# Performance work log

Hardware: AMD Instinct MI355X
Metric: run time of the kernel (lower is better)

The kernel has to match this reference:

```python
import jax, jax.numpy as jnp
import numpy as np

T, B, N, F = 128, 8, 32, 128
H = 256  # hidden channels
DEG = 8


def setup_inputs() -> dict:
    key = jax.random.key(0)
    ks = jax.random.split(key, 8)
    data = jax.random.normal(ks[0], (T, B, N, F), jnp.float32)
    all_ohs = jax.random.normal(ks[1], (T, B, N, 8), jnp.float32)
    n0 = B * N * T
    n1 = B * N * (T // 2)
    edge_index0 = jax.random.randint(ks[2], (2, n0 * DEG), 0, n0)
    edge_index1 = jax.random.randint(ks[3], (2, n1 * DEG), 0, n1)
    def init(k, shape, fan):
        return jax.random.normal(k, shape, jnp.float32) / np.float32(np.sqrt(fan))
    W0 = init(ks[4], (2 * F, H), 2 * F); b0 = jnp.zeros((H,), jnp.float32)
    Wc0 = init(ks[5], (H, H, 5), H * 5); bc0 = jnp.zeros((H,), jnp.float32)
    W1 = init(ks[6], (2 * H, H), 2 * H); b1 = jnp.zeros((H,), jnp.float32)
    Wc1 = init(ks[7], (H, H, 5), H * 5); bc1 = jnp.zeros((H,), jnp.float32)
    return dict(data=data, all_ohs=all_ohs,
                edge_index0=edge_index0, edge_index1=edge_index1,
                W0=W0, b0=b0, Wc0=Wc0, bc0=bc0,
                W1=W1, b1=b1, Wc1=Wc1, bc1=bc1)


def edge_conv(x, edge_index, W, b):
    # PyG EdgeConv: out_i = max_{(j->i)} relu(Linear(cat[x_i, x_j - x_i]))
    src, dst = edge_index[0], edge_index[1]
    x_i = x[dst]           # [E, C] target features
    x_j = x[src]           # [E, C] source features
    msg = jax.nn.relu(jnp.concatenate([x_i, x_j - x_i], axis=-1) @ W + b)
    out = jax.ops.segment_max(msg, dst, num_segments=x.shape[0])
    return jnp.where(jnp.isneginf(out), 0.0, out)  # empty segments -> 0 (PyG fill)


def temp_conv(x, Wc, bc):
    # x: [BN, C, L]; Conv1d(k=5, pad=2) + relu + MaxPool1d(2)
    y = jax.lax.conv_general_dilated(x, Wc, (1,), [(2, 2)],
                                     dimension_numbers=('NCH', 'OIH', 'NCH'))
    y = jax.nn.relu(y + bc[None, :, None])
    L2 = y.shape[-1] // 2
    y = y[..., : L2 * 2].reshape(y.shape[0], y.shape[1], L2, 2)
    return jnp.max(y, axis=-1)


def reference(data, all_ohs, edge_index0, edge_index1,
              W0, b0, Wc0, bc0, W1, b1, Wc1, bc1):
    # 'fast' path, context=False: all_ohs unused beyond reshape
    length = data.shape[0]
    x = data.reshape(T, B * N, F).transpose(1, 0, 2).reshape(-1, F)  # [BN*T, F]
    layers = ((edge_index0, W0, b0, Wc0, bc0),
              (edge_index1, W1, b1, Wc1, bc1))
    for ei, W, b, Wc, bc in layers:
        x = edge_conv(x, ei, W, b)                       # [BN*length, C]
        x = x.reshape(-1, length, x.shape[-1])           # [BN, length, C]
        x = x.transpose(0, 2, 1)                         # [BN, C, length]
        x = temp_conv(x, Wc, bc)                         # [BN, C, length//2]
        length = x.shape[2]
        C = x.shape[1]
        x = x.transpose(0, 2, 1).reshape(-1, C)          # [BN*length, C]
    return x
```

## Files before the change

kernel.cpp:

```cpp
#include <hip/hip_runtime.h>
#include <hip/hip_bf16.h>
#include <math.h>

#define T0 128
#define BN 256
#define Ff 128
#define Hh 256
#define NODE0 32768
#define E0 262144
#define T1 64
#define NODE1 16384
#define E1 131072
#define CAP 48

typedef __attribute__((ext_vector_type(8))) short bhalf8;
typedef __attribute__((ext_vector_type(4))) float floatx4;
typedef __attribute__((ext_vector_type(16))) float floatx16;

__device__ __forceinline__ unsigned short f2bf(float x) {
  union { float f; unsigned u; } v; v.f = x;
  unsigned r = v.u + 0x7fff + ((v.u >> 16) & 1);
  return (unsigned short)(r >> 16);
}
__device__ __forceinline__ float bf2f(unsigned short b) {
  union { unsigned u; float f; } v; v.u = ((unsigned)b) << 16;
  return v.f;
}
__device__ __forceinline__ void max2(float& mlo, float& mhi, int p) {
  union { unsigned u; float f; } lo, hi;
  lo.u = ((unsigned)p) << 16;
  hi.u = ((unsigned)p) & 0xffff0000u;
  mlo = fmaxf(mlo, lo.f);
  mhi = fmaxf(mhi, hi.f);
}

__global__ void k_prepfill(const float* __restrict__ data, unsigned short* __restrict__ X0b,
                           const float* __restrict__ W0, unsigned short* __restrict__ Wbot0,
                           unsigned short* __restrict__ Wd0,
                           const float* __restrict__ W1, unsigned short* __restrict__ Wbot1,
                           unsigned short* __restrict__ Wd1,
                           const float* __restrict__ Wc0, unsigned short* __restrict__ Wtb0,
                           const float* __restrict__ Wc1, unsigned short* __restrict__ Wtb1,
                           const int* __restrict__ ei0, const int* __restrict__ ei1,
                           int* __restrict__ cnt0, int* __restrict__ cnt1,
                           int* __restrict__ slot0, int* __restrict__ slot1) {
  int b = blockIdx.x;
  int tid = threadIdx.x;
  if (b < 2048) {
    int idx = b * 256 + tid;
    int c8 = idx & 15;
    int r  = idx >> 4;
    int t  = r & (T0 - 1);
    int bn = r >> 7;
    const float* s = data + ((size_t)t * BN + bn) * Ff + c8 * 8;
    float4 a = *(const float4*)s;
    float4 bb = *(const float4*)(s + 4);
    unsigned short o[8];
    o[0] = f2bf(a.x); o[1] = f2bf(a.y); o[2] = f2bf(a.z); o[3] = f2bf(a.w);
    o[4] = f2bf(bb.x); o[5] = f2bf(bb.y); o[6] = f2bf(bb.z); o[7] = f2bf(bb.w);
    *(int4*)(X0b + ((size_t)(bn * T0 + t) * Ff + c8 * 8)) = *(int4*)o;
  } else if (b < 2176) {
    int idx = (b - 2048) * 256 + tid;
    int n = idx >> 7, k = idx & 127;
    float top = W0[(size_t)k * 256 + n];
    float bot = W0[(size_t)(128 + k) * 256 + n];
    Wbot0[idx] = f2bf(bot);
    Wd0[idx]   = f2bf(top - bot);
  } else if (b < 2432) {
    int idx = (b - 2176) * 256 + tid;
    int n = idx >> 8, k = idx & 255;
    float top = W1[(size_t)k * 256 + n];
    float bot = W1[(size_t)(256 + k) * 256 + n];
    Wbot1[idx] = f2bf(bot);
    Wd1[idx]   = f2bf(top - bot);
  } else if (b < 3712) {
    int idx = (b - 2432) * 256 + tid;
    int tap = idx >> 16, o = (idx >> 8) & 255, i = idx & 255;
    Wtb0[idx] = f2bf(Wc0[((size_t)o * 256 + i) * 5 + tap]);
  } else if (b < 4992) {
    int idx = (b - 3712) * 256 + tid;
    int tap = idx >> 16, o = (idx >> 8) & 255, i = idx & 255;
    Wtb1[idx] = f2bf(Wc1[((size_t)o * 256 + i) * 5 + tap]);
  } else {
    int e = (b - 4992) * 256 + tid;
    if (e < E0) {
      int d = ei0[E0 + e];
      int p = atomicAdd(&cnt0[d], 1);
      if (p < CAP) slot0[(size_t)d * CAP + p] = ei0[e];
    } else {
      int e2 = e - E0;
      int d = ei1[E1 + e2];
      int p = atomicAdd(&cnt1[d], 1);
      if (p < CAP) slot1[(size_t)d * CAP + p] = ei1[e2];
    }
  }
}

__global__ __launch_bounds__(256) void k_gemm2(const unsigned short* __restrict__ A,
                                               const unsigned short* __restrict__ Wbot,
                                               const unsigned short* __restrict__ Wd,
                                               unsigned short* __restrict__ Bm,
                                               unsigned short* __restrict__ P, int K,
                                               const float* __restrict__ bias) {
  __shared__ __align__(16) short S_lds[3 * 128 * 72];
  short* A_lds  = S_lds;
  short* B0_lds = S_lds + 128 * 72;
  short* B1_lds = S_lds + 2 * 128 * 72;
  short* E_lds  = S_lds;
  int tid = threadIdx.x;
  int row0 = blockIdx.x * 128;
  int col0 = blockIdx.y * 128;
  int lane = tid & 63, wv = tid >> 6;
  int m16 = lane & 15, quad = lane >> 4;
  int sr = tid >> 3, sseg = tid & 7;

  floatx4 accB[2][8], accP[2][8];
#pragma unroll
  for (int rt = 0; rt < 2; ++rt)
#pragma unroll
    for (int nt = 0; nt < 8; ++nt) {
      accB[rt][nt] = (floatx4){0.f, 0.f, 0.f, 0.f};
      accP[rt][nt] = (floatx4){0.f, 0.f, 0.f, 0.f};
    }

  for (int kb = 0; kb < K; kb += 64) {
    __syncthreads();
#pragma unroll
    for (int i = 0; i < 4; ++i) {
      int r = sr + i * 32;
      *(int4*)&A_lds[r * 72 + sseg * 8] =
          *(const int4*)(A + (size_t)(row0 + r) * K + kb + sseg * 8);
      *(int4*)&B0_lds[r * 72 + sseg * 8] =
          *(const int4*)(Wbot + (size_t)(col0 + r) * K + kb + sseg * 8);
      *(int4*)&B1_lds[r * 72 + sseg * 8] =
          *(const int4*)(Wd + (size_t)(col0 + r) * K + kb + sseg * 8);
    }
    __syncthreads();
#pragma unroll
    for (int ks = 0; ks < 2; ++ks) {
      bhalf8 a0 = *(const bhalf8*)&A_lds[(wv * 32 + m16) * 72 + ks * 32 + quad * 8];
      bhalf8 a1 = *(const bhalf8*)&A_lds[(wv * 32 + 16 + m16) * 72 + ks * 32 + quad * 8];
#pragma unroll
      for (int nt = 0; nt < 8; ++nt) {
        bhalf8 b0 = *(const bhalf8*)&B0_lds[(nt * 16 + m16) * 72 + ks * 32 + quad * 8];
        accB[0][nt] = __builtin_amdgcn_mfma_f32_16x16x32_bf16(b0, a0, accB[0][nt], 0, 0, 0);
        accB[1][nt] = __builtin_amdgcn_mfma_f32_16x16x32_bf16(b0, a1, accB[1][nt], 0, 0, 0);
        bhalf8 b1 = *(const bhalf8*)&B1_lds[(nt * 16 + m16) * 72 + ks * 32 + quad * 8];
        accP[0][nt] = __builtin_amdgcn_mfma_f32_16x16x32_bf16(b1, a0, accP[0][nt], 0, 0, 0);
        accP[1][nt] = __builtin_amdgcn_mfma_f32_16x16x32_bf16(b1, a1, accP[1][nt], 0, 0, 0);
      }
    }
  }

  const int ESTR = 136;
  __syncthreads();

#pragma unroll
  for (int rt = 0; rt < 2; ++rt) {
    int lr = wv * 32 + rt * 16 + m16;
#pragma unroll
    for (int nt = 0; nt < 8; ++nt) {
      ushort4 ob;
      ob.x = f2bf(accB[rt][nt][0]); ob.y = f2bf(accB[rt][nt][1]);
      ob.z = f2bf(accB[rt][nt][2]); ob.w = f2bf(accB[rt][nt][3]);
      *(ushort4*)&E_lds[lr * ESTR + nt * 16 + quad * 4] = ob;
    }
  }
  __syncthreads();
#pragma unroll
  for (int i = 0; i < 8; ++i) {
    int u = tid + i * 256;
    int r = u >> 4, ch = u & 15;
    int4 v = *(const int4*)&E_lds[r * ESTR + ch * 8];
    *(int4*)(Bm + (size_t)(row0 + r) * 256 + col0 + ch * 8) = v;
  }
  __syncthreads();

#pragma unroll
  for (int rt = 0; rt < 2; ++rt) {
    int lr = wv * 32 + rt * 16 + m16;
#pragma unroll
    for (int nt = 0; nt < 8; ++nt) {
      int c = col0 + nt * 16 + quad * 4;
      float4 bv = *(const float4*)&bias[c];
      ushort4 op;
      op.x = f2bf(accP[rt][nt][0] + bv.x); op.y = f2bf(accP[rt][nt][1] + bv.y);
      op.z = f2bf(accP[rt][nt][2] + bv.z); op.w = f2bf(accP[rt][nt][3] + bv.w);
      *(ushort4*)&E_lds[lr * ESTR + nt * 16 + quad * 4] = op;
    }
  }
  __syncthreads();
#pragma unroll
  for (int i = 0; i < 8; ++i) {
    int u = tid + i * 256;
    int r = u >> 4, ch = u & 15;
    int4 v = *(const int4*)&E_lds[r * ESTR + ch * 8];
    *(int4*)(P + (size_t)(row0 + r) * 256 + col0 + ch * 8) = v;
  }
}

__global__ __launch_bounds__(256) void k_maxg2(const unsigned short* __restrict__ Bm,
                                               const int* __restrict__ cnt,
                                               const int* __restrict__ slot,
                                               const unsigned short* __restrict__ P,
                                               unsigned short* __restrict__ X1) {
  int node = blockIdx.x * 4 + (threadIdx.x >> 6);
  int lane = threadIdx.x & 63;
  int half = lane >> 5, c8 = lane & 31;
  int n = cnt[node];
  if (n > CAP) n = CAP;
  const int* sl = slot + (size_t)node * CAP;
  float m[8];
#pragma unroll
  for (int e = 0; e < 8; ++e) m[e] = -INFINITY;
  for (int i = 0; i < n; i += 8) {
    int s[4];
#pragma unroll
    for (int j = 0; j < 4; ++j) {
      int idx = i + 2 * j + half;
      s[j] = sl[(idx < n) ? idx : (n - 1)];
    }
    int4 v[4];
#pragma unroll
    for (int j = 0; j < 4; ++j)
      v[j] = *(const int4*)(Bm + (size_t)s[j] * 256 + c8 * 8);
#pragma unroll
    for (int j = 0; j < 4; ++j) {
      max2(m[0], m[1], v[j].x);
      max2(m[2], m[3], v[j].y);
      max2(m[4], m[5], v[j].z);
      max2(m[6], m[7], v[j].w);
    }
  }
#pragma unroll
  for (int e = 0; e < 8; ++e) m[e] = fmaxf(m[e], __shfl_xor(m[e], 32));
  if (half == 0) {
    int4 p = *(const int4*)(P + (size_t)node * 256 + c8 * 8);
    int4 o;
    unsigned short r0, r1;
    r0 = f2bf(fmaxf(bf2f((unsigned short)(p.x & 0xffff)) + m[0], 0.f));
    r1 = f2bf(fmaxf(bf2f((unsigned short)((unsigned)p.x >> 16)) + m[1], 0.f));
    o.x = (int)r0 | ((int)r1 << 16);
    r0 = f2bf(fmaxf(bf2f((unsigned short)(p.y & 0xffff)) + m[2], 0.f));
    r1 = f2bf(fmaxf(bf2f((unsigned short)((unsigned)p.y >> 16)) + m[3], 0.f));
    o.y = (int)r0 | ((int)r1 << 16);
    r0 = f2bf(fmaxf(bf2f((unsigned short)(p.z & 0xffff)) + m[4], 0.f));
    r1 = f2bf(fmaxf(bf2f((unsigned short)((unsigned)p.z >> 16)) + m[5], 0.f));
    o.z = (int)r0 | ((int)r1 << 16);
    r0 = f2bf(fmaxf(bf2f((unsigned short)(p.w & 0xffff)) + m[6], 0.f));
    r1 = f2bf(fmaxf(bf2f((unsigned short)((unsigned)p.w >> 16)) + m[7], 0.f));
    o.w = (int)r0 | ((int)r1 << 16);
    *(int4*)(X1 + (size_t)node * 256 + c8 * 8) = o;
  }
}

template <int TRows, int NT, bool OUT_F32>
__global__ __launch_bounds__(256) void k_conv32(const unsigned short* __restrict__ X,
                                                const unsigned short* __restrict__ Wtb,
                                                const float* __restrict__ bc,
                                                void* __restrict__ Yout) {
  const int CB = NT * 64;
  __shared__ __align__(16) short A_lds[2 * 68 * 40];
  __shared__ __align__(16) short B_lds[5 * CB * 40];
  int tid = threadIdx.x;
  int row0 = blockIdx.x * 128;
  int col0 = blockIdx.y * CB;
  int lane = tid & 63, wv = tid >> 6;
  int l31 = lane & 31, khalf = lane >> 5;
  int h = wv & 1, cpart = wv >> 1;

  floatx16 acc[2][NT];
#pragma unroll
  for (int rt = 0; rt < 2; ++rt)
#pragma unroll
    for (int ct = 0; ct < NT; ++ct)
#pragma unroll
      for (int r = 0; r < 16; ++r) acc[rt][ct][r] = 0.f;

  for (int kb = 0; kb < 256; kb += 32) {
    __syncthreads();
    for (int u = tid; u < 544; u += 256) {
      int s = (u >= 272) ? 1 : 0;
      int v = u - s * 272;
      int rr = v >> 2, seg = v & 3;
      int base = row0 + s * 64;
      int lo = base & ~(TRows - 1);
      int gr = base + rr - 2;
      int4 val = {0, 0, 0, 0};
      if (gr >= lo && gr < lo + TRows)
        val = *(const int4*)(X + (size_t)gr * 256 + kb + seg * 8);
      *(int4*)&A_lds[(s * 68 + rr) * 40 + seg * 8] = val;
    }
#pragma unroll
    for (int i = 0; i < 5 * NT; ++i) {
      int u = tid + i * 256;
      int r = u >> 2, seg = u & 3;
      int tap = r / CB, col = r % CB;
      *(int4*)&B_lds[r * 40 + seg * 8] =
          *(const int4*)(Wtb + (size_t)tap * 65536 + (size_t)(col0 + col) * 256 + kb + seg * 8);
    }
    __syncthreads();
#pragma unroll
    for (int tap = 0; tap < 5; ++tap) {
#pragma unroll
      for (int ks = 0; ks < 2; ++ks) {
        int ko = ks * 16 + khalf * 8;
        bhalf8 a[2];
#pragma unroll
        for (int rt = 0; rt < 2; ++rt)
          a[rt] = *(const bhalf8*)&A_lds[(h * 68 + rt * 32 + l31 + tap) * 40 + ko];
#pragma unroll
        for (int ct = 0; ct < NT; ++ct) {
          bhalf8 b = *(const bhalf8*)&B_lds[(tap * CB + cpart * NT * 32 + ct * 32 + l31) * 40 + ko];
#pragma unroll
          for (int rt = 0; rt < 2; ++rt)
            acc[rt][ct] = __builtin_amdgcn_mfma_f32_32x32x16_bf16(a[rt], b, acc[rt][ct], 0, 0, 0);
        }
      }
    }
  }

#pragma unroll
  for (int rt = 0; rt < 2; ++rt) {
#pragma unroll
    for (int ct = 0; ct < NT; ++ct) {
      int c = col0 + cpart * NT * 32 + ct * 32 + l31;
      float bv = bc[c];
#pragma unroll
      for (int r = 0; r < 16; r += 2) {
        int rowg = row0 + h * 64 + rt * 32 + 4 * khalf + 8 * (r >> 2) + (r & 3);
        float y0 = fmaxf(acc[rt][ct][r] + bv, 0.f);
        float y1 = fmaxf(acc[rt][ct][r + 1] + bv, 0.f);
        float p = fmaxf(y0, y1);
        int o = rowg >> 1;
        if (OUT_F32) ((float*)Yout)[(size_t)o * 256 + c] = p;
        else ((unsigned short*)Yout)[(size_t)o * 256 + c] = f2bf(p);
      }
    }
  }
}

extern "C" void kernel_launch(void* const* d_in, const int* in_sizes, int n_in,
                              void* d_out, int out_size, void* d_ws, size_t ws_size,
                              hipStream_t stream) {
  const float* data = (const float*)d_in[0];
  const int* ei0 = (const int*)d_in[2];
  const int* ei1 = (const int*)d_in[3];
  const float* W0  = (const float*)d_in[4];
  const float* b0  = (const float*)d_in[5];
  const float* Wc0 = (const float*)d_in[6];
  const float* bc0 = (const float*)d_in[7];
  const float* W1  = (const float*)d_in[8];
  const float* b1  = (const float*)d_in[9];
  const float* Wc1 = (const float*)d_in[10];
  const float* bc1 = (const float*)d_in[11];
  float* out = (float*)d_out;

  char* base = (char*)d_ws;
  size_t off = 0;
  auto alloc = [&](size_t bytes) { void* p = base + off; off += (bytes + 255) & ~(size_t)255; return p; };
  unsigned short* X0b   = (unsigned short*)alloc((size_t)NODE0 * Ff * 2);
  unsigned short* Bm    = (unsigned short*)alloc((size_t)NODE0 * Hh * 2);
  unsigned short* P     = (unsigned short*)alloc((size_t)NODE0 * Hh * 2);
  unsigned short* X1b   = (unsigned short*)alloc((size_t)NODE0 * Hh * 2);
  unsigned short* Y0b   = (unsigned short*)alloc((size_t)NODE1 * Hh * 2);
  unsigned short* Wbot0 = (unsigned short*)alloc(256 * 128 * 2);
  unsigned short* Wd0   = (unsigned short*)alloc(256 * 128 * 2);
  unsigned short* Wbot1 = (unsigned short*)alloc(256 * 256 * 2);
  unsigned short* Wd1   = (unsigned short*)alloc(256 * 256 * 2);
  unsigned short* Wtb0  = (unsigned short*)alloc(5 * 65536 * 2);
  unsigned short* Wtb1  = (unsigned short*)alloc(5 * 65536 * 2);
  int* cnt0  = (int*)alloc(NODE0 * 4);
  int* cnt1  = (int*)alloc(NODE1 * 4);
  int* slot0 = (int*)alloc((size_t)NODE0 * CAP * 4);
  int* slot1 = (int*)alloc((size_t)NODE1 * CAP * 4);

  hipMemsetAsync(cnt0, 0, (NODE0 + NODE1) * sizeof(int), stream);

  k_prepfill<<<6528, 256, 0, stream>>>(data, X0b, W0, Wbot0, Wd0, W1, Wbot1, Wd1,
                                       Wc0, Wtb0, Wc1, Wtb1,
                                       ei0, ei1, cnt0, cnt1, slot0, slot1);

  k_gemm2<<<dim3(NODE0 / 128, 2), 256, 0, stream>>>(X0b, Wbot0, Wd0, Bm, P, 128, b0);
  k_maxg2<<<NODE0 / 4, 256, 0, stream>>>(Bm, cnt0, slot0, P, X1b);
  k_conv32<128, 2, false><<<dim3(NODE0 / 128, 2), 256, 0, stream>>>(X1b, Wtb0, bc0, Y0b);

  k_gemm2<<<dim3(NODE1 / 128, 2), 256, 0, stream>>>(Y0b, Wbot1, Wd1, Bm, P, 256, b1);
  k_maxg2<<<NODE1 / 4, 256, 0, stream>>>(Bm, cnt1, slot1, P, X1b);
  k_conv32<64, 2, true><<<dim3(NODE1 / 128, 2), 256, 0, stream>>>(X1b, Wtb1, bc1, out);
}
```

Baseline: 220.0 us.

## Double-buffer conv LDS tiles via direct global-to-LDS loads with XOR swizzle

Rewrites the temporal conv kernel's staging. A and B tiles are now loaded with global_load_lds (16-byte direct-to-LDS) into two LDS buffers, so the next K-slice is fetched while MFMAs run on the current one. Row padding is replaced by an XOR swizzle of the 16-byte chunks to avoid bank conflicts. Out-of-range halo rows read from a zeroed scratch pad, which is cleared by extending the existing memset. This doubles the LDS footprint (about 100KB) and may lower occupancy.

```diff
diff --git a/kernel.cpp b/kernel.cpp
--- a/kernel.cpp
+++ b/kernel.cpp
@@ -32,6 +32,12 @@
   hi.u = ((unsigned)p) & 0xffff0000u;
   mlo = fmaxf(mlo, lo.f);
   mhi = fmaxf(mhi, hi.f);
+}
+
+__device__ __forceinline__ void gload16(const void* g, void* l) {
+  __builtin_amdgcn_global_load_lds(
+      (const __attribute__((address_space(1))) unsigned int*)g,
+      (__attribute__((address_space(3))) unsigned int*)l, 16, 0, 0);
 }
 
 __global__ void k_prepfill(const float* __restrict__ data, unsigned short* __restrict__ X0b,
@@ -254,77 +260,92 @@
   }
 }
 
-template <int TRows, int NT, bool OUT_F32>
+template <int TRows, bool OUT_F32>
 __global__ __launch_bounds__(256) void k_conv32(const unsigned short* __restrict__ X,
                                                 const unsigned short* __restrict__ Wtb,
                                                 const float* __restrict__ bc,
+                                                const unsigned short* __restrict__ zpad,
                                                 void* __restrict__ Yout) {
-  const int CB = NT * 64;
-  __shared__ __align__(16) short A_lds[2 * 68 * 40];
-  __shared__ __align__(16) short B_lds[5 * CB * 40];
+  __shared__ __align__(16) short LDS[2][800 * 32];
   int tid = threadIdx.x;
   int row0 = blockIdx.x * 128;
-  int col0 = blockIdx.y * CB;
+  int col0 = blockIdx.y * 128;
   int lane = tid & 63, wv = tid >> 6;
   int l31 = lane & 31, khalf = lane >> 5;
   int h = wv & 1, cpart = wv >> 1;
-
-  floatx16 acc[2][NT];
+  int lq = lane >> 2, lc = lane & 3;
+
+  floatx16 acc[2][2];
 #pragma unroll
   for (int rt = 0; rt < 2; ++rt)
 #pragma unroll
-    for (int ct = 0; ct < NT; ++ct)
+    for (int ct = 0; ct < 2; ++ct)
 #pragma unroll
       for (int r = 0; r < 16; ++r) acc[rt][ct][r] = 0.f;
 
-  for (int kb = 0; kb < 256; kb += 32) {
-    __syncthreads();
-    for (int u = tid; u < 544; u += 256) {
-      int s = (u >= 272) ? 1 : 0;
-      int v = u - s * 272;
-      int rr = v >> 2, seg = v & 3;
-      int base = row0 + s * 64;
-      int lo = base & ~(TRows - 1);
-      int gr = base + rr - 2;
-      int4 val = {0, 0, 0, 0};
-      if (gr >= lo && gr < lo + TRows)
-        val = *(const int4*)(X + (size_t)gr * 256 + kb + seg * 8);
-      *(int4*)&A_lds[(s * 68 + rr) * 40 + seg * 8] = val;
-    }
-#pragma unroll
-    for (int i = 0; i < 5 * NT; ++i) {
-      int u = tid + i * 256;
-      int r = u >> 2, seg = u & 3;
-      int tap = r / CB, col = r % CB;
-      *(int4*)&B_lds[r * 40 + seg * 8] =
-          *(const int4*)(Wtb + (size_t)tap * 65536 + (size_t)(col0 + col) * 256 + kb + seg * 8);
-    }
-    __syncthreads();
+  auto stage = [&](int buf, int kb) {
+    for (int i = wv; i < 50; i += 4) {
+      const unsigned short* src;
+      int rho0;
+      if (i < 10) {
+        int s = (i >= 5) ? 1 : 0;
+        int j = i - s * 5;
+        rho0 = s * 80 + j * 16;
+        int r = j * 16 + lq;
+        int rho = rho0 + lq;
+        int cs = lc ^ ((rho >> 1) & 3);
+        int gr = row0 + s * 64 - 2 + r;
+        int lo = (row0 + s * 64) & ~(TRows - 1);
+        bool ok = (r < 68) && (gr >= lo) && (gr < lo + TRows);
+        src = ok ? (X + (size_t)gr * 256 + kb + cs * 8) : (zpad + lc * 8);
+      } else {
+        int j = i - 10;
+        rho0 = 160 + j * 16;
+        int v = j * 16 + lq;
+        int rho = rho0 + lq;
+        int cs = lc ^ ((rho >> 1) & 3);
+        int tap = v >> 7, col = v & 127;
+        src = Wtb + (size_t)tap * 65536 + (size_t)(col0 + col) * 256 + kb + cs * 8;
+      }
+      gload16(src, &LDS[buf][rho0 * 32]);
+    }
+  };
+
+  stage(0, 0);
+  __syncthreads();
+  int cur = 0;
+  for (int t = 0; t < 8; ++t) {
+    if (t < 7) stage(cur ^ 1, (t + 1) * 32);
 #pragma unroll
     for (int tap = 0; tap < 5; ++tap) {
 #pragma unroll
       for (int ks = 0; ks < 2; ++ks) {
-        int ko = ks * 16 + khalf * 8;
+        int c = ks * 2 + khalf;
         bhalf8 a[2];
 #pragma unroll
-        for (int rt = 0; rt < 2; ++rt)
-          a[rt] = *(const bhalf8*)&A_lds[(h * 68 + rt * 32 + l31 + tap) * 40 + ko];
-#pragma unroll
-        for (int ct = 0; ct < NT; ++ct) {
-          bhalf8 b = *(const bhalf8*)&B_lds[(tap * CB + cpart * NT * 32 + ct * 32 + l31) * 40 + ko];
+        for (int rt = 0; rt < 2; ++rt) {
+          int rho = h * 80 + rt * 32 + l31 + tap;
+          a[rt] = *(const bhalf8*)&LDS[cur][rho * 32 + ((c ^ ((rho >> 1) & 3)) * 8)];
+        }
+#pragma unroll
+        for (int ct = 0; ct < 2; ++ct) {
+          int rho = 160 + tap * 128 + cpart * 64 + ct * 32 + l31;
+          bhalf8 b = *(const bhalf8*)&LDS[cur][rho * 32 + ((c ^ ((rho >> 1) & 3)) * 8)];
 #pragma unroll
           for (int rt = 0; rt < 2; ++rt)
             acc[rt][ct] = __builtin_amdgcn_mfma_f32_32x32x16_bf16(a[rt], b, acc[rt][ct], 0, 0, 0);
         }
       }
     }
+    __syncthreads();
+    cur ^= 1;
   }
 
 #pragma unroll
   for (int rt = 0; rt < 2; ++rt) {
 #pragma unroll
-    for (int ct = 0; ct < NT; ++ct) {
-      int c = col0 + cpart * NT * 32 + ct * 32 + l31;
+    for (int ct = 0; ct < 2; ++ct) {
+      int c = col0 + cpart * 64 + ct * 32 + l31;
       float bv = bc[c];
 #pragma unroll
       for (int r = 0; r < 16; r += 2) {
@@ -372,10 +393,11 @@
   unsigned short* Wtb1  = (unsigned short*)alloc(5 * 65536 * 2);
   int* cnt0  = (int*)alloc(NODE0 * 4);
   int* cnt1  = (int*)alloc(NODE1 * 4);
+  unsigned short* zpad = (unsigned short*)alloc(256);
   int* slot0 = (int*)alloc((size_t)NODE0 * CAP * 4);
   int* slot1 = (int*)alloc((size_t)NODE1 * CAP * 4);
 
-  hipMemsetAsync(cnt0, 0, (NODE0 + NODE1) * sizeof(int), stream);
+  hipMemsetAsync(cnt0, 0, (NODE0 + NODE1) * sizeof(int) + 256, stream);
 
   k_prepfill<<<6528, 256, 0, stream>>>(data, X0b, W0, Wbot0, Wd0, W1, Wbot1, Wd1,
                                        Wc0, Wtb0, Wc1, Wtb1,
@@ -383,9 +405,9 @@
 
   k_gemm2<<<dim3(NODE0 / 128, 2), 256, 0, stream>>>(X0b, Wbot0, Wd0, Bm, P, 128, b0);
   k_maxg2<<<NODE0 / 4, 256, 0, stream>>>(Bm, cnt0, slot0, P, X1b);
-  k_conv32<128, 2, false><<<dim3(NODE0 / 128, 2), 256, 0, stream>>>(X1b, Wtb0, bc0, Y0b);
+  k_conv32<128, false><<<dim3(NODE0 / 128, 2), 256, 0, stream>>>(X1b, Wtb0, bc0, zpad, Y0b);
 
   k_gemm2<<<dim3(NODE1 / 128, 2), 256, 0, stream>>>(Y0b, Wbot1, Wd1, Bm, P, 256, b1);
   k_maxg2<<<NODE1 / 4, 256, 0, stream>>>(Bm, cnt1, slot1, P, X1b);
-  k_conv32<64, 2, true><<<dim3(NODE1 / 128, 2), 256, 0, stream>>>(X1b, Wtb1, bc1, out);
-}
+  k_conv32<64, true><<<dim3(NODE1 / 128, 2), 256, 0, stream>>>(X1b, Wtb1, bc1, zpad, out);
+}
```

Result: slower. 240.3 us (+9.2%).
